# Kernel optimization log

Measured on AMD Instinct MI355X. Metric: run time of the kernel, lower is better.

## Reference

```python
import jax, jax.numpy as jnp
import numpy as np

B = 8192          # num_envs
OPT = 16          # num options
SHARED = 22       # shared_state_size (hardcoded in module)
UNIQ = 8          # unique_state_size (hardcoded in module)
MIN_DUR, MAX_DUR = 0.1, 0.5  # const.gait_net.valid_swing_duration_range


def _w(k, o, i):
    return jax.random.normal(k, (o, i), jnp.float32) * (1.0 / np.sqrt(i))


def setup_inputs() -> dict:
    key = jax.random.key(0)
    ks = jax.random.split(key, 20)
    obs = jax.random.normal(ks[0], (B, SHARED + OPT * UNIQ), jnp.float32)
    flag = jax.random.uniform(ks[1], (B, OPT)) < 0.25
    u = obs[:, SHARED:].reshape(B, OPT, UNIQ)
    u = u.at[:, :, 0].set(jnp.where(flag, 1.0, u[:, :, 0]))
    obs = jnp.concatenate([obs[:, :SHARED], u.reshape(B, OPT * UNIQ)], axis=1)
    return {
        "obs": obs,
        "sw1": _w(ks[2], 256, 22), "sb1": jnp.zeros((256,), jnp.float32),
        "sw2": _w(ks[3], 256, 256), "sb2": jnp.zeros((256,), jnp.float32),
        "uw1": _w(ks[4], 128, 8), "ub1": jnp.zeros((128,), jnp.float32),
        "uw2": _w(ks[5], 128, 128), "ub2": jnp.zeros((128,), jnp.float32),
        "no_op_embedding": jax.random.normal(ks[6], (128,), jnp.float32),
        "tw1": _w(ks[7], 512, 384), "tb1": jnp.zeros((512,), jnp.float32),
        "tw2": _w(ks[8], 256, 512), "tb2": jnp.zeros((256,), jnp.float32),
        "vw": _w(ks[9], 1, 256), "vb": jnp.zeros((1,), jnp.float32),
        "dw": _w(ks[10], 1, 256), "db": jnp.zeros((1,), jnp.float32),
    }


def reference(obs, sw1, sb1, sw2, sb2, uw1, ub1, uw2, ub2, no_op_embedding,
              tw1, tb1, tw2, tb2, vw, vb, dw, db):
    relu = jax.nn.relu
    shared = obs[:, :SHARED]                               # [B, 22]
    uniq = obs[:, SHARED:].reshape(B, OPT, UNIQ)           # [B, OPT, 8]
    # shared encoder (22 -> 256 -> 256, relu output)
    se = relu(relu(shared @ sw1.T + sb1) @ sw2.T + sb2)    # [B, 256]
    # unique encoder applied to all options at once (8 -> 128 -> 128)
    ue = relu(relu(uniq @ uw1.T + ub1) @ uw2.T + ub2)      # [B, OPT, 128]
    no_op = uniq[:, :, 0] == 1.0                           # [B, OPT]
    ue = jnp.where(no_op[..., None], no_op_embedding, ue)
    trunk_in = jnp.concatenate(
        [jnp.broadcast_to(se[:, None, :], (B, OPT, se.shape[-1])), ue], axis=-1)
    t = relu(relu(trunk_in @ tw1.T + tb1) @ tw2.T + tb2)   # [B, OPT, 256]
    logits = (t @ vw.T + vb).squeeze(-1)                   # [B, OPT]
    duration = jax.nn.sigmoid((t @ dw.T + db).squeeze(-1)) * (MAX_DUR - MIN_DUR) + MIN_DUR
    return logits, duration
```

## Files before the change

kernel.cpp:

```cpp
#include <hip/hip_runtime.h>
#include <stdint.h>


static constexpr int B_ = 8192;

typedef __attribute__((ext_vector_type(8))) short bf16x8;
typedef __attribute__((ext_vector_type(4))) float f32x4;

__device__ __forceinline__ float u2f(uint16_t u) {
    union { uint32_t i; float f; } c; c.i = (uint32_t)u << 16; return c.f;
}
__device__ __forceinline__ uint16_t f2u(float f) {
    __bf16 b = (__bf16)f;
    return __builtin_bit_cast(uint16_t, b);
}

static constexpr size_t WCSE   = 0;
static constexpr size_t WTW1SE = 4194304;
static constexpr size_t WTW1UE = WTW1SE + 131072;
static constexpr size_t WTW2   = WTW1UE + 65536;
static constexpr size_t WUW2   = WTW2 + 131072;
static constexpr size_t WSW2   = WUW2 + 16384;
static constexpr size_t WUW1B  = WSW2 + 65536;

__global__ __launch_bounds__(256) void k_conv(
    const float* __restrict__ tw1, const float* __restrict__ tw2,
    const float* __restrict__ uw2, const float* __restrict__ sw2,
    const float* __restrict__ uw1, uint16_t* __restrict__ ws)
{
    int i4 = blockIdx.x * 256 + threadIdx.x;
    if (i4 >= 102400) {
        int q = i4 - 102400;
        int n = q >> 3, k0 = (q & 7) * 4;
        ushort4 o = {0, 0, 0, 0};
        if (k0 < 8) {
            float4 v = *reinterpret_cast<const float4*>(uw1 + n * 8 + k0);
            o.x = f2u(v.x); o.y = f2u(v.y); o.z = f2u(v.z); o.w = f2u(v.w);
        }
        *reinterpret_cast<ushort4*>(ws + WUW1B + n * 32 + k0) = o;
        return;
    }
    const float* src; size_t dst;
    if (i4 < 32768) {
        int g = i4 * 4, n = g >> 8, k = g & 255;
        src = tw1 + (size_t)n * 384 + k;
        dst = WTW1SE + (size_t)g;
    } else if (i4 < 49152) {
        int q = i4 - 32768, n = q >> 5, w = q & 31;
        src = tw1 + (size_t)n * 384 + 256 + w * 4;
        dst = WTW1UE + (size_t)n * 128 + w * 4;
    } else if (i4 < 81920) {
        int q = (i4 - 49152) * 4;
        src = tw2 + q; dst = WTW2 + q;
    } else if (i4 < 86016) {
        int q = (i4 - 81920) * 4;
        src = uw2 + q; dst = WUW2 + q;
    } else {
        int q = (i4 - 86016) * 4;
        src = sw2 + q; dst = WSW2 + q;
    }
    float4 v = *reinterpret_cast<const float4*>(src);
    ushort4 o;
    o.x = f2u(v.x); o.y = f2u(v.y); o.z = f2u(v.z); o.w = f2u(v.w);
    *reinterpret_cast<ushort4*>(ws + dst) = o;
}

__global__ __launch_bounds__(512) void k_cse(
    const float* __restrict__ obs,
    const float* __restrict__ sw1, const float* __restrict__ sb1,
    const float* __restrict__ sb2, const float* __restrict__ tb1,
    uint16_t* __restrict__ ws)
{
    __shared__ float xs[16][24];
    __shared__ uint16_t h1s[16 * 264];
    __shared__ uint16_t seL[16 * 264];
    const int t = threadIdx.x;
    const int b0 = blockIdx.x * 16;
    const uint16_t* sw2b   = ws + WSW2;
    const uint16_t* tw1seb = ws + WTW1SE;

    if (t < 352) {
        int e = t / 22, c = t - e * 22;
        xs[e][c] = obs[(size_t)(b0 + e) * 150 + c];
    }
    __syncthreads();
    {
        const int n = t & 255;
        float w[22];
        #pragma unroll
        for (int k = 0; k < 22; ++k) w[k] = sw1[n * 22 + k];
        const float bias = sb1[n];
        #pragma unroll
        for (int ii = 0; ii < 8; ++ii) {
            int e = (t >> 8) * 8 + ii;
            float a = bias;
            #pragma unroll
            for (int k = 0; k < 22; ++k) a += w[k] * xs[e][k];
            h1s[e * 264 + n] = f2u(fmaxf(a, 0.f));
        }
    }
    __syncthreads();
    const int wv = t >> 6, lane = t & 63, quad = lane >> 4, l16 = lane & 15;
    {
        f32x4 acc[2];
        #pragma unroll
        for (int nt = 0; nt < 2; ++nt) {
            float bv = sb2[wv * 32 + nt * 16 + l16];
            acc[nt] = {bv, bv, bv, bv};
        }
        const uint16_t* bb = sw2b + (size_t)(wv * 32 + l16) * 256 + quad * 8;
        bf16x8 bc[2], bn[2];
        bc[0] = *reinterpret_cast<const bf16x8*>(bb);
        bc[1] = *reinterpret_cast<const bf16x8*>(bb + 4096);
        #pragma unroll
        for (int kk = 0; kk < 8; ++kk) {
            if (kk < 7) {
                bn[0] = *reinterpret_cast<const bf16x8*>(bb + (kk + 1) * 32);
                bn[1] = *reinterpret_cast<const bf16x8*>(bb + 4096 + (kk + 1) * 32);
            }
            bf16x8 af = *reinterpret_cast<const bf16x8*>(
                &h1s[l16 * 264 + kk * 32 + quad * 8]);
            #pragma unroll
            for (int nt = 0; nt < 2; ++nt)
                acc[nt] = __builtin_amdgcn_mfma_f32_16x16x32_bf16(
                    af, bc[nt], acc[nt], 0, 0, 0);
            bc[0] = bn[0]; bc[1] = bn[1];
        }
        #pragma unroll
        for (int nt = 0; nt < 2; ++nt)
            #pragma unroll
            for (int r = 0; r < 4; ++r)
                seL[(quad * 4 + r) * 264 + wv * 32 + nt * 16 + l16] =
                    f2u(fmaxf(acc[nt][r], 0.f));
    }
    __syncthreads();
    {
        f32x4 acc[4];
        #pragma unroll
        for (int nt = 0; nt < 4; ++nt) {
            float bv = tb1[wv * 64 + nt * 16 + l16];
            acc[nt] = {bv, bv, bv, bv};
        }
        const uint16_t* bb = tw1seb + (size_t)(wv * 64 + l16) * 256 + quad * 8;
        bf16x8 bc[4], bn[4];
        #pragma unroll
        for (int nt = 0; nt < 4; ++nt)
            bc[nt] = *reinterpret_cast<const bf16x8*>(bb + nt * 4096);
        #pragma unroll
        for (int kk = 0; kk < 8; ++kk) {
            if (kk < 7) {
                #pragma unroll
                for (int nt = 0; nt < 4; ++nt)
                    bn[nt] = *reinterpret_cast<const bf16x8*>(
                        bb + nt * 4096 + (kk + 1) * 32);
            }
            bf16x8 af = *reinterpret_cast<const bf16x8*>(
                &seL[l16 * 264 + kk * 32 + quad * 8]);
            #pragma unroll
            for (int nt = 0; nt < 4; ++nt)
                acc[nt] = __builtin_amdgcn_mfma_f32_16x16x32_bf16(
                    af, bc[nt], acc[nt], 0, 0, 0);
            #pragma unroll
            for (int nt = 0; nt < 4; ++nt) bc[nt] = bn[nt];
        }
        #pragma unroll
        for (int nt = 0; nt < 4; ++nt)
            #pragma unroll
            for (int r = 0; r < 4; ++r)
                ws[WCSE + (size_t)(b0 + quad * 4 + r) * 512 +
                   wv * 64 + nt * 16 + l16] = f2u(acc[nt][r]);
    }
}

static constexpr int UQB_OFF  = 0;
static constexpr int NOOP_OFF = 5120;
static constexpr int CSE_OFF  = 5376;
static constexpr int H1U_OFF  = 9472;
static constexpr int UET_OFF  = 26880;
static constexpr int H1T_OFF  = 44288;
static constexpr int SMEM_SZ  = 78080;

__global__ __launch_bounds__(512, 4) void k_main(
    const float* __restrict__ obs,
    const float* __restrict__ ub1,
    const float* __restrict__ ub2, const float* __restrict__ emb,
    const float* __restrict__ tb2,
    const float* __restrict__ vw,  const float* __restrict__ vb,
    const float* __restrict__ dw,  const float* __restrict__ db,
    const uint16_t* __restrict__ wsb,
    float* __restrict__ out)
{
    __shared__ __align__(16) char smem[SMEM_SZ];
    uint16_t* uqb   = (uint16_t*)(smem + UQB_OFF);
    float*    noopf = (float*)(smem + NOOP_OFF);
    uint16_t* cseL  = (uint16_t*)(smem + CSE_OFF);
    uint16_t* h1u   = (uint16_t*)(smem + H1U_OFF);
    uint16_t* uet   = (uint16_t*)(smem + UET_OFF);
    uint16_t* h1t   = (uint16_t*)(smem + H1T_OFF);
    uint16_t* t2    = h1t;

    const int t    = threadIdx.x;
    const int wv   = t >> 6;
    const int lane = t & 63;
    const int quad = lane >> 4;
    const int l16  = lane & 15;
    const int b0   = blockIdx.x * 4;

    const uint16_t* csep  = wsb + WCSE;
    const uint16_t* tw1ue = wsb + WTW1UE;
    const uint16_t* tw2b  = wsb + WTW2;
    const uint16_t* uw2b  = wsb + WUW2;
    const uint16_t* uw1b  = wsb + WUW1B;

    {
        int r = t >> 3, q = t & 7;
        int e = r >> 4, o = r & 15;
        ushort4 ov = {0, 0, 0, 0};
        if (q < 2) {
            const float2* sp = reinterpret_cast<const float2*>(
                &obs[(size_t)(b0 + e) * 150 + 22 + o * 8 + q * 4]);
            float2 a = sp[0], b = sp[1];
            ov.x = f2u(a.x); ov.y = f2u(a.y); ov.z = f2u(b.x); ov.w = f2u(b.y);
        }
        *reinterpret_cast<ushort4*>(&uqb[r * 40 + q * 4]) = ov;
        #pragma unroll
        for (int ii = 0; ii < 2; ++ii) {
            int i = t + ii * 512;
            int ee = i >> 8, cc = i & 255;
            ((uint32_t*)cseL)[ee * 256 + cc] =
                ((const uint32_t*)(csep + (size_t)(b0 + ee) * 512))[cc];
        }
        if (t < 64) {
            int ee = t >> 4, oo = t & 15;
            noopf[t] = (obs[(size_t)(b0 + ee) * 150 + 22 + oo * 8] == 1.0f) ? 1.0f : 0.0f;
        }
    }
    __syncthreads();

    {
        const int n = wv * 16 + l16;
        const float bv = ub1[n];
        f32x4 acc[4];
        #pragma unroll
        for (int mt = 0; mt < 4; ++mt) acc[mt] = {bv, bv, bv, bv};
        bf16x8 bf = *reinterpret_cast<const bf16x8*>(&uw1b[n * 32 + quad * 8]);
        #pragma unroll
        for (int mt = 0; mt < 4; ++mt) {
            bf16x8 af = *reinterpret_cast<const bf16x8*>(
                &uqb[(mt * 16 + l16) * 40 + quad * 8]);
            acc[mt] = __builtin_amdgcn_mfma_f32_16x16x32_bf16(af, bf, acc[mt], 0, 0, 0);
        }
        #pragma unroll
        for (int mt = 0; mt < 4; ++mt)
            #pragma unroll
            for (int r = 0; r < 4; ++r) {
                int row = mt * 16 + quad * 4 + r;
                h1u[row * 136 + n] = f2u(fmaxf(acc[mt][r], 0.f));
            }
    }
    __syncthreads();

    {
        const int n = wv * 16 + l16;
        const float bv = ub2[n];
        const float ev = emb[n];
        f32x4 acc[4];
        #pragma unroll
        for (int mt = 0; mt < 4; ++mt) acc[mt] = {bv, bv, bv, bv};
        #pragma unroll
        for (int kk = 0; kk < 4; ++kk) {
            bf16x8 bf = *reinterpret_cast<const bf16x8*>(
                &uw2b[(size_t)n * 128 + kk * 32 + quad * 8]);
            #pragma unroll
            for (int mt = 0; mt < 4; ++mt) {
                bf16x8 af = *reinterpret_cast<const bf16x8*>(
                    &h1u[(mt * 16 + l16) * 136 + kk * 32 + quad * 8]);
                acc[mt] = __builtin_amdgcn_mfma_f32_16x16x32_bf16(af, bf, acc[mt], 0, 0, 0);
            }
        }
        #pragma unroll
        for (int mt = 0; mt < 4; ++mt)
            #pragma unroll
            for (int r = 0; r < 4; ++r) {
                int row = mt * 16 + quad * 4 + r;
                float v = (noopf[row] != 0.0f) ? ev : fmaxf(acc[mt][r], 0.f);
                uet[row * 136 + n] = f2u(v);
            }
    }
    __syncthreads();

    f32x4 acc2[4][2];
    #pragma unroll
    for (int nt = 0; nt < 2; ++nt) {
        float bv = tb2[wv * 32 + nt * 16 + l16];
        #pragma unroll
        for (int mt = 0; mt < 4; ++mt) acc2[mt][nt] = {bv, bv, bv, bv};
    }

    #pragma unroll
    for (int nc = 0; nc < 2; ++nc) {
        {
            f32x4 acc1[4][2];
            #pragma unroll
            for (int nt = 0; nt < 2; ++nt) {
                int n = nc * 256 + wv * 32 + nt * 16 + l16;
                #pragma unroll
                for (int mt = 0; mt < 4; ++mt) {
                    float v = u2f(cseL[mt * 512 + n]);
                    acc1[mt][nt] = {v, v, v, v};
                }
            }
            const uint16_t* bb = tw1ue + (size_t)(nc * 256 + wv * 32 + l16) * 128
                                 + quad * 8;
            bf16x8 bc[2], bn[2];
            bc[0] = *reinterpret_cast<const bf16x8*>(bb);
            bc[1] = *reinterpret_cast<const bf16x8*>(bb + 2048);
            #pragma unroll
            for (int kk = 0; kk < 4; ++kk) {
                if (kk < 3) {
                    bn[0] = *reinterpret_cast<const bf16x8*>(bb + (kk + 1) * 32);
                    bn[1] = *reinterpret_cast<const bf16x8*>(bb + 2048 + (kk + 1) * 32);
                }
                bf16x8 af[4];
                #pragma unroll
                for (int mt = 0; mt < 4; ++mt)
                    af[mt] = *reinterpret_cast<const bf16x8*>(
                        &uet[(mt * 16 + l16) * 136 + kk * 32 + quad * 8]);
                #pragma unroll
                for (int mt = 0; mt < 4; ++mt)
                    #pragma unroll
                    for (int nt = 0; nt < 2; ++nt)
                        acc1[mt][nt] = __builtin_amdgcn_mfma_f32_16x16x32_bf16(
                            af[mt], bc[nt], acc1[mt][nt], 0, 0, 0);
                bc[0] = bn[0]; bc[1] = bn[1];
            }
            #pragma unroll
            for (int mt = 0; mt < 4; ++mt)
                #pragma unroll
                for (int nt = 0; nt < 2; ++nt)
                    #pragma unroll
                    for (int r = 0; r < 4; ++r) {
                        int row = mt * 16 + quad * 4 + r;
                        h1t[row * 264 + wv * 32 + nt * 16 + l16] =
                            f2u(fmaxf(acc1[mt][nt][r], 0.f));
                    }
        }
        __syncthreads();
        {
            const uint16_t* cb = tw2b + (size_t)(wv * 32 + l16) * 512 + nc * 256
                                 + quad * 8;
            bf16x8 cc[2], cn[2];
            cc[0] = *reinterpret_cast<const bf16x8*>(cb);
            cc[1] = *reinterpret_cast<const bf16x8*>(cb + 8192);
            #pragma unroll
            for (int k2 = 0; k2 < 8; ++k2) {
                if (k2 < 7) {
                    cn[0] = *reinterpret_cast<const bf16x8*>(cb + (k2 + 1) * 32);
                    cn[1] = *reinterpret_cast<const bf16x8*>(cb + 8192 + (k2 + 1) * 32);
                }
                bf16x8 af[4];
                #pragma unroll
                for (int mt = 0; mt < 4; ++mt)
                    af[mt] = *reinterpret_cast<const bf16x8*>(
                        &h1t[(mt * 16 + l16) * 264 + k2 * 32 + quad * 8]);
                #pragma unroll
                for (int mt = 0; mt < 4; ++mt)
                    #pragma unroll
                    for (int nt = 0; nt < 2; ++nt)
                        acc2[mt][nt] = __builtin_amdgcn_mfma_f32_16x16x32_bf16(
                            af[mt], cc[nt], acc2[mt][nt], 0, 0, 0);
                cc[0] = cn[0]; cc[1] = cn[1];
            }
        }
        if (nc == 0) __syncthreads();
    }
    __syncthreads();
    #pragma unroll
    for (int mt = 0; mt < 4; ++mt)
        #pragma unroll
        for (int nt = 0; nt < 2; ++nt)
            #pragma unroll
            for (int r = 0; r < 4; ++r) {
                int row = mt * 16 + quad * 4 + r;
                t2[row * 264 + wv * 32 + nt * 16 + l16] =
                    f2u(fmaxf(acc2[mt][nt][r], 0.f));
            }
    __syncthreads();

    {
        float vwf[4], dwf[4];
        #pragma unroll
        for (int j = 0; j < 4; ++j) {
            vwf[j] = vw[lane + 64 * j];
            dwf[j] = dw[lane + 64 * j];
        }
        const float vbf = vb[0], dbf = db[0];
        #pragma unroll
        for (int rr = 0; rr < 8; ++rr) {
            int row = wv * 8 + rr;
            float sv = 0.f, sd = 0.f;
            #pragma unroll
            for (int j = 0; j < 4; ++j) {
                float tv = u2f(t2[row * 264 + lane + 64 * j]);
                sv += tv * vwf[j];
                sd += tv * dwf[j];
            }
            #pragma unroll
            for (int off = 32; off > 0; off >>= 1) {
                sv += __shfl_down(sv, off);
                sd += __shfl_down(sd, off);
            }
            if (lane == 0) {
                int g = blockIdx.x * 64 + row;
                out[g] = sv + vbf;
                float z = sd + dbf;
                float sig = 1.f / (1.f + __expf(-z));
                out[B_ * 16 + g] = sig * 0.4f + 0.1f;
            }
        }
    }
}

extern "C" void kernel_launch(void* const* d_in, const int* in_sizes, int n_in,
                              void* d_out, int out_size, void* d_ws, size_t ws_size,
                              hipStream_t stream) {
    const float* obs = (const float*)d_in[0];
    const float* sw1 = (const float*)d_in[1];
    const float* sb1 = (const float*)d_in[2];
    const float* sw2 = (const float*)d_in[3];
    const float* sb2 = (const float*)d_in[4];
    const float* uw1 = (const float*)d_in[5];
    const float* ub1 = (const float*)d_in[6];
    const float* uw2 = (const float*)d_in[7];
    const float* ub2 = (const float*)d_in[8];
    const float* emb = (const float*)d_in[9];
    const float* tw1 = (const float*)d_in[10];
    const float* tb1 = (const float*)d_in[11];
    const float* tw2 = (const float*)d_in[12];
    const float* tb2 = (const float*)d_in[13];
    const float* vw  = (const float*)d_in[14];
    const float* vb  = (const float*)d_in[15];
    const float* dw  = (const float*)d_in[16];
    const float* db  = (const float*)d_in[17];

    uint16_t* wsb = (uint16_t*)d_ws;

    k_conv<<<404, 256, 0, stream>>>(tw1, tw2, uw2, sw2, uw1, wsb);
    k_cse<<<512, 512, 0, stream>>>(obs, sw1, sb1, sb2, tb1, wsb);
    k_main<<<B_ / 4, 512, 0, stream>>>(obs, ub1, ub2, emb, tb2,
                                       vw, vb, dw, db, wsb, (float*)d_out);
}
```

Baseline: 236.6 us.

## Fuse weight conversion into shared-encoder kernel and read fp32 weights directly

```diff
diff --git a/kernel.cpp b/kernel.cpp
--- a/kernel.cpp
+++ b/kernel.cpp
@@ -13,6 +13,14 @@
 __device__ __forceinline__ uint16_t f2u(float f) {
     __bf16 b = (__bf16)f;
     return __builtin_bit_cast(uint16_t, b);
+}
+__device__ __forceinline__ bf16x8 cvt8(float4 a, float4 b) {
+    bf16x8 r;
+    r[0] = (short)f2u(a.x); r[1] = (short)f2u(a.y);
+    r[2] = (short)f2u(a.z); r[3] = (short)f2u(a.w);
+    r[4] = (short)f2u(b.x); r[5] = (short)f2u(b.y);
+    r[6] = (short)f2u(b.z); r[7] = (short)f2u(b.w);
+    return r;
 }
 
 static constexpr size_t WCSE   = 0;
@@ -23,52 +31,13 @@
 static constexpr size_t WSW2   = WUW2 + 16384;
 static constexpr size_t WUW1B  = WSW2 + 65536;
 
-__global__ __launch_bounds__(256) void k_conv(
-    const float* __restrict__ tw1, const float* __restrict__ tw2,
-    const float* __restrict__ uw2, const float* __restrict__ sw2,
-    const float* __restrict__ uw1, uint16_t* __restrict__ ws)
-{
-    int i4 = blockIdx.x * 256 + threadIdx.x;
-    if (i4 >= 102400) {
-        int q = i4 - 102400;
-        int n = q >> 3, k0 = (q & 7) * 4;
-        ushort4 o = {0, 0, 0, 0};
-        if (k0 < 8) {
-            float4 v = *reinterpret_cast<const float4*>(uw1 + n * 8 + k0);
-            o.x = f2u(v.x); o.y = f2u(v.y); o.z = f2u(v.z); o.w = f2u(v.w);
-        }
-        *reinterpret_cast<ushort4*>(ws + WUW1B + n * 32 + k0) = o;
-        return;
-    }
-    const float* src; size_t dst;
-    if (i4 < 32768) {
-        int g = i4 * 4, n = g >> 8, k = g & 255;
-        src = tw1 + (size_t)n * 384 + k;
-        dst = WTW1SE + (size_t)g;
-    } else if (i4 < 49152) {
-        int q = i4 - 32768, n = q >> 5, w = q & 31;
-        src = tw1 + (size_t)n * 384 + 256 + w * 4;
-        dst = WTW1UE + (size_t)n * 128 + w * 4;
-    } else if (i4 < 81920) {
-        int q = (i4 - 49152) * 4;
-        src = tw2 + q; dst = WTW2 + q;
-    } else if (i4 < 86016) {
-        int q = (i4 - 81920) * 4;
-        src = uw2 + q; dst = WUW2 + q;
-    } else {
-        int q = (i4 - 86016) * 4;
-        src = sw2 + q; dst = WSW2 + q;
-    }
-    float4 v = *reinterpret_cast<const float4*>(src);
-    ushort4 o;
-    o.x = f2u(v.x); o.y = f2u(v.y); o.z = f2u(v.z); o.w = f2u(v.w);
-    *reinterpret_cast<ushort4*>(ws + dst) = o;
-}
-
-__global__ __launch_bounds__(512) void k_cse(
+__global__ __launch_bounds__(512) void k_cse_conv(
     const float* __restrict__ obs,
     const float* __restrict__ sw1, const float* __restrict__ sb1,
-    const float* __restrict__ sb2, const float* __restrict__ tb1,
+    const float* __restrict__ sw2, const float* __restrict__ sb2,
+    const float* __restrict__ tw1, const float* __restrict__ tb1,
+    const float* __restrict__ tw2, const float* __restrict__ uw2,
+    const float* __restrict__ uw1,
     uint16_t* __restrict__ ws)
 {
     __shared__ float xs[16][24];
@@ -76,8 +45,39 @@
     __shared__ uint16_t seL[16 * 264];
     const int t = threadIdx.x;
     const int b0 = blockIdx.x * 16;
-    const uint16_t* sw2b   = ws + WSW2;
-    const uint16_t* tw1seb = ws + WTW1SE;
+
+    if (t < 106) {
+        int j = blockIdx.x * 106 + t;
+        if (j < 16384) {
+            int n = j >> 5, w = j & 31;
+            float4 v = *reinterpret_cast<const float4*>(
+                tw1 + (size_t)n * 384 + 256 + w * 4);
+            ushort4 o;
+            o.x = f2u(v.x); o.y = f2u(v.y); o.z = f2u(v.z); o.w = f2u(v.w);
+            *reinterpret_cast<ushort4*>(ws + WTW1UE + (size_t)n * 128 + w * 4) = o;
+        } else if (j < 49152) {
+            int q = (j - 16384) * 4;
+            float4 v = *reinterpret_cast<const float4*>(tw2 + q);
+            ushort4 o;
+            o.x = f2u(v.x); o.y = f2u(v.y); o.z = f2u(v.z); o.w = f2u(v.w);
+            *reinterpret_cast<ushort4*>(ws + WTW2 + q) = o;
+        } else if (j < 53248) {
+            int q = (j - 49152) * 4;
+            float4 v = *reinterpret_cast<const float4*>(uw2 + q);
+            ushort4 o;
+            o.x = f2u(v.x); o.y = f2u(v.y); o.z = f2u(v.z); o.w = f2u(v.w);
+            *reinterpret_cast<ushort4*>(ws + WUW2 + q) = o;
+        } else {
+            int q = j - 53248;
+            int n = q >> 3, k0 = (q & 7) * 4;
+            ushort4 o = {0, 0, 0, 0};
+            if (k0 < 8) {
+                float4 v = *reinterpret_cast<const float4*>(uw1 + n * 8 + k0);
+                o.x = f2u(v.x); o.y = f2u(v.y); o.z = f2u(v.z); o.w = f2u(v.w);
+            }
+            *reinterpret_cast<ushort4*>(ws + WUW1B + n * 32 + k0) = o;
+        }
+    }
 
     if (t < 352) {
         int e = t / 22, c = t - e * 22;
@@ -108,23 +108,19 @@
             float bv = sb2[wv * 32 + nt * 16 + l16];
             acc[nt] = {bv, bv, bv, bv};
         }
-        const uint16_t* bb = sw2b + (size_t)(wv * 32 + l16) * 256 + quad * 8;
-        bf16x8 bc[2], bn[2];
-        bc[0] = *reinterpret_cast<const bf16x8*>(bb);
-        bc[1] = *reinterpret_cast<const bf16x8*>(bb + 4096);
+        const float* bb = sw2 + (size_t)(wv * 32 + l16) * 256 + quad * 8;
         #pragma unroll
         for (int kk = 0; kk < 8; ++kk) {
-            if (kk < 7) {
-                bn[0] = *reinterpret_cast<const bf16x8*>(bb + (kk + 1) * 32);
-                bn[1] = *reinterpret_cast<const bf16x8*>(bb + 4096 + (kk + 1) * 32);
-            }
             bf16x8 af = *reinterpret_cast<const bf16x8*>(
                 &h1s[l16 * 264 + kk * 32 + quad * 8]);
             #pragma unroll
-            for (int nt = 0; nt < 2; ++nt)
+            for (int nt = 0; nt < 2; ++nt) {
+                const float* p = bb + nt * 4096 + kk * 32;
+                float4 a = *reinterpret_cast<const float4*>(p);
+                float4 b = *reinterpret_cast<const float4*>(p + 4);
                 acc[nt] = __builtin_amdgcn_mfma_f32_16x16x32_bf16(
-                    af, bc[nt], acc[nt], 0, 0, 0);
-            bc[0] = bn[0]; bc[1] = bn[1];
+                    af, cvt8(a, b), acc[nt], 0, 0, 0);
+            }
         }
         #pragma unroll
         for (int nt = 0; nt < 2; ++nt)
@@ -135,40 +131,35 @@
     }
     __syncthreads();
     {
-        f32x4 acc[4];
-        #pragma unroll
-        for (int nt = 0; nt < 4; ++nt) {
-            float bv = tb1[wv * 64 + nt * 16 + l16];
-            acc[nt] = {bv, bv, bv, bv};
-        }
-        const uint16_t* bb = tw1seb + (size_t)(wv * 64 + l16) * 256 + quad * 8;
-        bf16x8 bc[4], bn[4];
-        #pragma unroll
-        for (int nt = 0; nt < 4; ++nt)
-            bc[nt] = *reinterpret_cast<const bf16x8*>(bb + nt * 4096);
-        #pragma unroll
-        for (int kk = 0; kk < 8; ++kk) {
-            if (kk < 7) {
-                #pragma unroll
-                for (int nt = 0; nt < 4; ++nt)
-                    bn[nt] = *reinterpret_cast<const bf16x8*>(
-                        bb + nt * 4096 + (kk + 1) * 32);
-            }
-            bf16x8 af = *reinterpret_cast<const bf16x8*>(
-                &seL[l16 * 264 + kk * 32 + quad * 8]);
-            #pragma unroll
-            for (int nt = 0; nt < 4; ++nt)
-                acc[nt] = __builtin_amdgcn_mfma_f32_16x16x32_bf16(
-                    af, bc[nt], acc[nt], 0, 0, 0);
-            #pragma unroll
-            for (int nt = 0; nt < 4; ++nt) bc[nt] = bn[nt];
-        }
-        #pragma unroll
-        for (int nt = 0; nt < 4; ++nt)
-            #pragma unroll
-            for (int r = 0; r < 4; ++r)
-                ws[WCSE + (size_t)(b0 + quad * 4 + r) * 512 +
-                   wv * 64 + nt * 16 + l16] = f2u(acc[nt][r]);
+        const float* bb = tw1 + (size_t)(wv * 64 + l16) * 384 + quad * 8;
+        #pragma unroll
+        for (int h = 0; h < 2; ++h) {
+            f32x4 acc[2];
+            #pragma unroll
+            for (int nt2 = 0; nt2 < 2; ++nt2) {
+                float bv = tb1[wv * 64 + (h * 2 + nt2) * 16 + l16];
+                acc[nt2] = {bv, bv, bv, bv};
+            }
+            #pragma unroll
+            for (int kk = 0; kk < 8; ++kk) {
+                bf16x8 af = *reinterpret_cast<const bf16x8*>(
+                    &seL[l16 * 264 + kk * 32 + quad * 8]);
+                #pragma unroll
+                for (int nt2 = 0; nt2 < 2; ++nt2) {
+                    const float* p = bb + (size_t)(h * 2 + nt2) * 6144 + kk * 32;
+                    float4 a = *reinterpret_cast<const float4*>(p);
+                    float4 b = *reinterpret_cast<const float4*>(p + 4);
+                    acc[nt2] = __builtin_amdgcn_mfma_f32_16x16x32_bf16(
+                        af, cvt8(a, b), acc[nt2], 0, 0, 0);
+                }
+            }
+            #pragma unroll
+            for (int nt2 = 0; nt2 < 2; ++nt2)
+                #pragma unroll
+                for (int r = 0; r < 4; ++r)
+                    ws[WCSE + (size_t)(b0 + quad * 4 + r) * 512 +
+                       wv * 64 + (h * 2 + nt2) * 16 + l16] = f2u(acc[nt2][r]);
+        }
     }
 }
 
@@ -445,8 +436,8 @@
 
     uint16_t* wsb = (uint16_t*)d_ws;
 
-    k_conv<<<404, 256, 0, stream>>>(tw1, tw2, uw2, sw2, uw1, wsb);
-    k_cse<<<512, 512, 0, stream>>>(obs, sw1, sb1, sb2, tb1, wsb);
+    k_cse_conv<<<512, 512, 0, stream>>>(obs, sw1, sb1, sw2, sb2, tw1, tb1,
+                                        tw2, uw2, uw1, wsb);
     k_main<<<B_ / 4, 512, 0, stream>>>(obs, ub1, ub2, emb, tb2,
                                        vw, vb, dw, db, wsb, (float*)d_out);
 }
```

Measured after the change: 255.0 us. +7.7%, slower.
